# Performance work log

Hardware: AMD Instinct MI355X
Metric: run time of the kernel (lower is better)

## Reference

```python
import jax, jax.numpy as jnp
import numpy as np

DIM = 128
NUM_HEADS = 4
HEAD_DIM = DIM // NUM_HEADS
WH, WW = 7, 7
N_TOK = WH * WW
LAMBDA_K = 1.0
TEMP_MAX = 4.0


def _relative_position_index(wh, ww):
    coords = np.stack(np.meshgrid(np.arange(wh), np.arange(ww), indexing='ij'))  # [2,wh,ww]
    flat = coords.reshape(2, -1)                         # [2,N]
    rel = flat[:, :, None] - flat[:, None, :]            # [2,N,N]
    rel = rel.transpose(1, 2, 0).copy()                  # [N,N,2]
    rel[:, :, 0] += wh - 1
    rel[:, :, 1] += ww - 1
    rel[:, :, 0] *= 2 * ww - 1
    return rel.sum(-1).astype(np.int32)                  # [N,N]


def setup_inputs() -> dict:
    key = jax.random.key(0)
    ks = jax.random.split(key, 10)
    B = 4096
    x = jax.random.normal(ks[0], (B, N_TOK, DIM), dtype=jnp.float32)
    token_u_temp = jax.random.normal(ks[1], (B, N_TOK), dtype=jnp.float32)
    token_u_bias = jax.random.normal(ks[2], (B, N_TOK), dtype=jnp.float32)
    token_gate = jax.random.uniform(ks[3], (B, NUM_HEADS, N_TOK), dtype=jnp.float32)
    qkv_w = jax.random.normal(ks[4], (3 * DIM, DIM), dtype=jnp.float32) * (DIM ** -0.5)
    qkv_b = jax.random.normal(ks[5], (3 * DIM,), dtype=jnp.float32) * 0.02
    proj_w = jax.random.normal(ks[6], (DIM, DIM), dtype=jnp.float32) * (DIM ** -0.5)
    proj_b = jax.random.normal(ks[7], (DIM,), dtype=jnp.float32) * 0.02
    rel_table = jax.random.normal(ks[8], ((2 * WH - 1) * (2 * WW - 1), NUM_HEADS), dtype=jnp.float32) * 0.02
    rel_index = jnp.asarray(_relative_position_index(WH, WW))
    return {
        'x': x, 'token_u_temp': token_u_temp, 'token_u_bias': token_u_bias,
        'token_gate': token_gate, 'qkv_w': qkv_w, 'qkv_b': qkv_b,
        'proj_w': proj_w, 'proj_b': proj_b, 'rel_table': rel_table,
        'rel_index': rel_index,
    }


def reference(x, token_u_temp, token_u_bias, token_gate, qkv_w, qkv_b, proj_w, proj_b, rel_table, rel_index):
    B, N, C = x.shape
    qkv = x @ qkv_w.T + qkv_b                             # [B,N,3C]
    qkv = qkv.reshape(B, N, 3, NUM_HEADS, HEAD_DIM).transpose(2, 0, 3, 1, 4)
    q, k, v = qkv[0], qkv[1], qkv[2]                      # [B,H,N,hd]
    # per-token temperature scaling of q
    T = 0.1 + TEMP_MAX * jax.nn.sigmoid(token_u_temp)     # [B,N]
    q = q / T[:, None, :, None]
    # gathered relative-position bias + per-key bias penalty
    bias = rel_table[rel_index.reshape(-1)].reshape(N, N, NUM_HEADS)
    bias = bias.transpose(2, 0, 1)[None]                  # [1,H,N,N]
    uB = jax.nn.relu(token_u_bias)                        # [B,N]
    mask = bias - LAMBDA_K * uB[:, None, None, :]         # [B,H,N,N]
    scores = jnp.einsum('bhnd,bhmd->bhnm', q, k) * (HEAD_DIM ** -0.5) + mask
    attn = jax.nn.softmax(scores, axis=-1)
    out = jnp.einsum('bhnm,bhmd->bhnd', attn, v)          # [B,H,N,hd]
    out = out * token_gate[:, :, :, None]                 # per-token, per-head gate
    out = out.transpose(0, 2, 1, 3).reshape(B, N, C)
    return out @ proj_w.T + proj_b
```

## Files before the change

kernel.cpp:

```cpp
#include <hip/hip_runtime.h>

typedef short s8v __attribute__((ext_vector_type(8)));
typedef float f4v __attribute__((ext_vector_type(4)));

#define NTOK 49
#define LDS_Q    0
#define LDS_K    6468
#define LDS_RT   12936
#define LDS_UB   12985
#define LDS_GATE 13034
#define LDS_TOT  13230

#define WS_BIAS_OFF 262144

__device__ __forceinline__ unsigned short f2bf(float f){
    unsigned x = __float_as_uint(f);
    x += 0x7fffu + ((x >> 16) & 1u);
    return (unsigned short)(x >> 16);
}
__device__ __forceinline__ void split8t(const float* f, s8v& hi, s8v& lo){
    #pragma unroll
    for (int j = 0; j < 8; ++j){
        unsigned u = __float_as_uint(f[j]);
        hi[j] = (short)(u >> 16);
        float r = f[j] - __uint_as_float(u & 0xffff0000u);
        lo[j] = (short)(__float_as_uint(r) >> 16);
    }
}

__global__ void prep_kernel(const float* __restrict__ qkv_w, const float* __restrict__ proj_w,
                            const float* __restrict__ rel_table, const int* __restrict__ rel_index,
                            void* __restrict__ ws){
    int i = blockIdx.x * 256 + threadIdx.x;
    unsigned short* qh = (unsigned short*)ws;
    unsigned short* ql = qh + 49152;
    unsigned short* ph = (unsigned short*)((char*)ws + 196608);
    unsigned short* pl = (unsigned short*)((char*)ws + 229376);
    float* biasT = (float*)((char*)ws + WS_BIAS_OFF);
    if (i < 49152){
        float v = qkv_w[i];
        unsigned u = __float_as_uint(v);
        qh[i] = (unsigned short)(u >> 16);
        ql[i] = (unsigned short)(__float_as_uint(v - __uint_as_float(u & 0xffff0000u)) >> 16);
    } else if (i < 65536){
        int j = i - 49152;
        float v = proj_w[j];
        unsigned u = __float_as_uint(v);
        ph[j] = (unsigned short)(u >> 16);
        pl[j] = (unsigned short)(__float_as_uint(v - __uint_as_float(u & 0xffff0000u)) >> 16);
    } else if (i < 75140){
        int j = i - 65536;
        int h = j / 2401, r = j % 2401;
        biasT[h*2401 + r] = rel_table[rel_index[r]*4 + h];
    }
}

#define MFMA(a,b,c) __builtin_amdgcn_mfma_f32_16x16x32_bf16((a),(b),(c),0,0,0)

__global__ __launch_bounds__(256, 3)
void win_attn(const float* __restrict__ x, const float* __restrict__ u_temp,
              const float* __restrict__ u_bias, const float* __restrict__ gate,
              const float* __restrict__ qkv_b, const float* __restrict__ proj_b,
              const void* __restrict__ ws, float* __restrict__ out)
{
    __shared__ float sm[LDS_TOT];
    const int b = blockIdx.x, tid = threadIdx.x;
    const int l  = tid & 63;
    const int w  = __builtin_amdgcn_readfirstlane(tid >> 6);
    const int lc = l & 15, q4 = l >> 4;

    if (tid < NTOK){
        float u  = u_temp[b*NTOK + tid];
        float sg = 1.f / (1.f + __expf(-u));
        sm[LDS_RT + tid] = 0.17677669529663687f / (0.1f + 4.f*sg);
        float ub = u_bias[b*NTOK + tid];
        sm[LDS_UB + tid] = ub > 0.f ? ub : 0.f;
    }
    if (tid < 196) sm[LDS_GATE + tid] = gate[b*196 + tid];
    __syncthreads();

    const unsigned short* qkh = (const unsigned short*)ws;
    const unsigned short* qkl = qkh + 49152;

    f4v vhold[2][4];
    #pragma unroll
    for (int mp = 0; mp < 2; ++mp){
        s8v ah[2][4], al[2][4];
        #pragma unroll
        for (int m2 = 0; m2 < 2; ++m2){
            int row = (mp*2 + m2)*16 + lc; if (row > 48) row = 48;
            const float* xp = x + ((size_t)b*NTOK + row)*128 + q4*8;
            #pragma unroll
            for (int kf = 0; kf < 4; ++kf){
                float xv[8];
                float4 t0 = *(const float4*)(xp + kf*32);
                float4 t1 = *(const float4*)(xp + kf*32 + 4);
                xv[0]=t0.x; xv[1]=t0.y; xv[2]=t0.z; xv[3]=t0.w;
                xv[4]=t1.x; xv[5]=t1.y; xv[6]=t1.z; xv[7]=t1.w;
                split8t(xv, ah[m2][kf], al[m2][kf]);
            }
        }
        #pragma unroll
        for (int g = 0; g < 3; ++g){
            #pragma unroll
            for (int t = 0; t < 2; ++t){
                int nt  = (g==0 ? 2*w : (g==1 ? 8+2*w : 16+2*w)) + t;
                int col = nt*16 + lc;
                s8v bh[4], bl[4];
                #pragma unroll
                for (int kf = 0; kf < 4; ++kf){
                    int off = col*128 + kf*32 + q4*8;
                    bh[kf] = *(const s8v*)(qkh + off);
                    bl[kf] = *(const s8v*)(qkl + off);
                }
                float bia = qkv_b[col];
                #pragma unroll
                for (int m2 = 0; m2 < 2; ++m2){
                    f4v acc = {bia, bia, bia, bia};
                    #pragma unroll
                    for (int kf = 0; kf < 4; ++kf){
                        acc = MFMA(ah[m2][kf], bh[kf], acc);
                        acc = MFMA(ah[m2][kf], bl[kf], acc);
                        acc = MFMA(al[m2][kf], bh[kf], acc);
                    }
                    int mt = mp*2 + m2;
                    if (g == 2){
                        vhold[t][mt] = acc;
                    } else {
                        #pragma unroll
                        for (int r = 0; r < 4; ++r){
                            int row = mt*16 + q4*4 + r;
                            if (row < NTOK){
                                if (g == 0) sm[LDS_Q + row*132 + col] = acc[r] * sm[LDS_RT + row];
                                else        sm[LDS_K + row*132 + (col - 128)] = acc[r];
                            }
                        }
                    }
                }
            }
        }
    }

    s8v Kh[4], Kl[4], Qh[4], Ql[4];
    #pragma unroll
    for (int t = 0; t < 4; ++t){
        int row = 16*t + lc; if (row > 48) row = 48;
        float fv[8];
        {
            const float* p = &sm[LDS_K + row*132 + w*32 + q4*8];
            float4 a0 = *(const float4*)p; float4 a1 = *(const float4*)(p + 4);
            fv[0]=a0.x; fv[1]=a0.y; fv[2]=a0.z; fv[3]=a0.w;
            fv[4]=a1.x; fv[5]=a1.y; fv[6]=a1.z; fv[7]=a1.w;
            split8t(fv, Kh[t], Kl[t]);
        }
        {
            const float* p = &sm[LDS_Q + row*132 + w*32 + q4*8];
            float4 a0 = *(const float4*)p; float4 a1 = *(const float4*)(p + 4);
            fv[0]=a0.x; fv[1]=a0.y; fv[2]=a0.z; fv[3]=a0.w;
            fv[4]=a1.x; fv[5]=a1.y; fv[6]=a1.z; fv[7]=a1.w;
            split8t(fv, Qh[t], Ql[t]);
        }
    }

    const float* biasT = (const float*)((const char*)ws + WS_BIAS_OFF);
    unsigned short* P = (unsigned short*)sm;
    #pragma unroll
    for (int nt = 0; nt < 4; ++nt){
        int qy = nt*16 + lc;
        int qyc = qy > 48 ? 48 : qy;
        f4v S[4];
        #pragma unroll
        for (int mt = 0; mt < 4; ++mt){
            f4v a;
            #pragma unroll
            for (int r = 0; r < 4; ++r){
                int ky = mt*16 + q4*4 + r; if (ky > 48) ky = 48;
                a[r] = biasT[w*2401 + qyc*49 + ky] - sm[LDS_UB + ky];
            }
            a = MFMA(Kh[mt], Qh[nt], a);
            a = MFMA(Kh[mt], Ql[nt], a);
            a = MFMA(Kl[mt], Qh[nt], a);
            S[mt] = a;
        }
        #pragma unroll
        for (int r = 0; r < 4; ++r){
            int ky = 48 + q4*4 + r;
            if (ky >= NTOK) S[3][r] = -1e30f;
        }
        float mx = -3e38f;
        #pragma unroll
        for (int mt = 0; mt < 4; ++mt)
            #pragma unroll
            for (int r = 0; r < 4; ++r) mx = fmaxf(mx, S[mt][r]);
        mx = fmaxf(mx, __shfl_xor(mx, 16));
        mx = fmaxf(mx, __shfl_xor(mx, 32));
        float sum = 0.f;
        #pragma unroll
        for (int mt = 0; mt < 4; ++mt)
            #pragma unroll
            for (int r = 0; r < 4; ++r){
                float e = __expf(S[mt][r] - mx);
                S[mt][r] = e; sum += e;
            }
        sum += __shfl_xor(sum, 16);
        sum += __shfl_xor(sum, 32);
        float rs = 1.f / sum;
        if (qy < NTOK){
            #pragma unroll
            for (int mt = 0; mt < 4; ++mt)
                #pragma unroll
                for (int r = 0; r < 4; ++r){
                    int ky = mt*16 + q4*4 + r;
                    P[(qy*132 + w*32)*2 + (((ky>>3) ^ (qy&7)) << 3) + (ky&7)] = f2bf(S[mt][r] * rs);
                }
        }
    }

    #pragma unroll
    for (int t = 0; t < 2; ++t)
        #pragma unroll
        for (int mt = 0; mt < 4; ++mt)
            #pragma unroll
            for (int r = 0; r < 4; ++r){
                int row = mt*16 + q4*4 + r;
                if (row < NTOK) sm[LDS_K + row*132 + w*32 + t*16 + lc] = vhold[t][mt][r];
            }

    s8v Pa[4][2];
    #pragma unroll
    for (int mt = 0; mt < 4; ++mt)
        #pragma unroll
        for (int kf = 0; kf < 2; ++kf){
            int qy = mt*16 + lc; if (qy > 48) qy = 48;
            int ch = (4*kf + q4) ^ (qy & 7);
            Pa[mt][kf] = *(const s8v*)(P + (qy*132 + w*32)*2 + ch*8);
        }
    s8v Vb[2][2];
    #pragma unroll
    for (int t = 0; t < 2; ++t)
        #pragma unroll
        for (int kf = 0; kf < 2; ++kf){
            #pragma unroll
            for (int j = 0; j < 8; ++j){
                int key = kf*32 + q4*8 + j; if (key > 48) key = 48;
                Vb[t][kf][j] = (short)(__float_as_uint(sm[LDS_K + key*132 + w*32 + t*16 + lc]) >> 16);
            }
        }
    f4v O[4][2];
    #pragma unroll
    for (int mt = 0; mt < 4; ++mt)
        #pragma unroll
        for (int t = 0; t < 2; ++t){
            f4v o = {0.f, 0.f, 0.f, 0.f};
            o = MFMA(Pa[mt][0], Vb[t][0], o);
            o = MFMA(Pa[mt][1], Vb[t][1], o);
            O[mt][t] = o;
        }

    #pragma unroll
    for (int mt = 0; mt < 4; ++mt)
        #pragma unroll
        for (int t = 0; t < 2; ++t)
            #pragma unroll
            for (int r = 0; r < 4; ++r){
                int row = mt*16 + q4*4 + r;
                if (row < NTOK){
                    float vg = O[mt][t][r] * sm[LDS_GATE + w*49 + row];
                    unsigned u = __float_as_uint(vg);
                    float res = vg - __uint_as_float(u & 0xffff0000u);
                    char* bp = (char*)sm + (LDS_K + row*132 + w*32)*4;
                    ((unsigned short*)bp)[t*16 + lc]        = (unsigned short)(u >> 16);
                    ((unsigned short*)(bp + 64))[t*16 + lc] = (unsigned short)(__float_as_uint(res) >> 16);
                }
            }
    __syncthreads();

    const unsigned short* ph = (const unsigned short*)((const char*)ws + 196608);
    const unsigned short* pl = (const unsigned short*)((const char*)ws + 229376);
    s8v Bh[2][4], Bl[2][4];
    #pragma unroll
    for (int t = 0; t < 2; ++t){
        int col = (2*w + t)*16 + lc;
        #pragma unroll
        for (int kf = 0; kf < 4; ++kf){
            int off = col*128 + kf*32 + q4*8;
            Bh[t][kf] = *(const s8v*)(ph + off);
            Bl[t][kf] = *(const s8v*)(pl + off);
        }
    }
    #pragma unroll
    for (int mt = 0; mt < 4; ++mt){
        int row = mt*16 + lc; if (row > 48) row = 48;
        s8v Ah[4], Al[4];
        #pragma unroll
        for (int kf = 0; kf < 4; ++kf){
            const char* bp = (const char*)sm + (LDS_K + row*132 + kf*32)*4;
            Ah[kf] = *(const s8v*)(bp + q4*16);
            Al[kf] = *(const s8v*)(bp + 64 + q4*16);
        }
        #pragma unroll
        for (int t = 0; t < 2; ++t){
            int col = (2*w + t)*16 + lc;
            float bia = proj_b[col];
            f4v acc = {bia, bia, bia, bia};
            #pragma unroll
            for (int kf = 0; kf < 4; ++kf){
                acc = MFMA(Ah[kf], Bh[t][kf], acc);
                acc = MFMA(Ah[kf], Bl[t][kf], acc);
                acc = MFMA(Al[kf], Bh[t][kf], acc);
            }
            #pragma unroll
            for (int r = 0; r < 4; ++r){
                int r2 = mt*16 + q4*4 + r;
                if (r2 < NTOK) out[((size_t)b*NTOK + r2)*128 + col] = acc[r];
            }
        }
    }
}

extern "C" void kernel_launch(void* const* d_in, const int* in_sizes, int n_in,
                              void* d_out, int out_size, void* d_ws, size_t ws_size,
                              hipStream_t stream) {
    const float* x  = (const float*)d_in[0];
    const float* ut = (const float*)d_in[1];
    const float* ub = (const float*)d_in[2];
    const float* tg = (const float*)d_in[3];
    const float* qw = (const float*)d_in[4];
    const float* qb = (const float*)d_in[5];
    const float* pw = (const float*)d_in[6];
    const float* pb = (const float*)d_in[7];
    const float* rt = (const float*)d_in[8];
    const int*   ri = (const int*)d_in[9];
    float* o = (float*)d_out;
    const int B = in_sizes[0] / (NTOK * 128);

    prep_kernel<<<294, 256, 0, stream>>>(qw, pw, rt, ri, d_ws);
    win_attn<<<B, 256, 0, stream>>>(x, ut, ub, tg, qb, pb, d_ws, o);
}
```

Before: 496.8 us.

## Double-buffer QKV weight loads, transpose bias table, hoist proj weight loads

```diff
diff --git a/kernel.cpp b/kernel.cpp
--- a/kernel.cpp
+++ b/kernel.cpp
@@ -51,13 +51,13 @@
     } else if (i < 75140){
         int j = i - 65536;
         int h = j / 2401, r = j % 2401;
-        biasT[h*2401 + r] = rel_table[rel_index[r]*4 + h];
+        biasT[h*2401 + (r % 49)*49 + (r / 49)] = rel_table[rel_index[r]*4 + h];
     }
 }
 
 #define MFMA(a,b,c) __builtin_amdgcn_mfma_f32_16x16x32_bf16((a),(b),(c),0,0,0)
 
-__global__ __launch_bounds__(256, 3)
+__global__ __launch_bounds__(256, 2)
 void win_attn(const float* __restrict__ x, const float* __restrict__ u_temp,
               const float* __restrict__ u_bias, const float* __restrict__ gate,
               const float* __restrict__ qkv_b, const float* __restrict__ proj_b,
@@ -100,40 +100,54 @@
                 split8t(xv, ah[m2][kf], al[m2][kf]);
             }
         }
-        #pragma unroll
-        for (int g = 0; g < 3; ++g){
-            #pragma unroll
-            for (int t = 0; t < 2; ++t){
-                int nt  = (g==0 ? 2*w : (g==1 ? 8+2*w : 16+2*w)) + t;
-                int col = nt*16 + lc;
-                s8v bh[4], bl[4];
+        s8v bhA[4], blA[4], bhB[4], blB[4];
+        {
+            int col = (2*w)*16 + lc;
+            #pragma unroll
+            for (int kf = 0; kf < 4; ++kf){
+                int off = col*128 + kf*32 + q4*8;
+                bhA[kf] = *(const s8v*)(qkh + off);
+                blA[kf] = *(const s8v*)(qkl + off);
+            }
+        }
+        #pragma unroll
+        for (int idx = 0; idx < 6; ++idx){
+            const int g = idx >> 1, t = idx & 1;
+            int nt  = (g==0 ? 2*w : (g==1 ? 8+2*w : 16+2*w)) + t;
+            int col = nt*16 + lc;
+            if (idx < 5){
+                const int g2 = (idx+1) >> 1, t2 = (idx+1) & 1;
+                int nt2  = (g2==0 ? 2*w : (g2==1 ? 8+2*w : 16+2*w)) + t2;
+                int col2 = nt2*16 + lc;
                 #pragma unroll
                 for (int kf = 0; kf < 4; ++kf){
-                    int off = col*128 + kf*32 + q4*8;
-                    bh[kf] = *(const s8v*)(qkh + off);
-                    bl[kf] = *(const s8v*)(qkl + off);
-                }
-                float bia = qkv_b[col];
+                    int off = col2*128 + kf*32 + q4*8;
+                    if (idx & 1){ bhA[kf] = *(const s8v*)(qkh + off); blA[kf] = *(const s8v*)(qkl + off); }
+                    else        { bhB[kf] = *(const s8v*)(qkh + off); blB[kf] = *(const s8v*)(qkl + off); }
+                }
+            }
+            float bia = qkv_b[col];
+            #pragma unroll
+            for (int m2 = 0; m2 < 2; ++m2){
+                f4v acc = {bia, bia, bia, bia};
                 #pragma unroll
-                for (int m2 = 0; m2 < 2; ++m2){
-                    f4v acc = {bia, bia, bia, bia};
+                for (int kf = 0; kf < 4; ++kf){
+                    s8v bh = (idx & 1) ? bhB[kf] : bhA[kf];
+                    s8v bl = (idx & 1) ? blB[kf] : blA[kf];
+                    acc = MFMA(ah[m2][kf], bh, acc);
+                    acc = MFMA(ah[m2][kf], bl, acc);
+                    acc = MFMA(al[m2][kf], bh, acc);
+                }
+                int mt = mp*2 + m2;
+                if (g == 2){
+                    vhold[t][mt] = acc;
+                } else {
                     #pragma unroll
-                    for (int kf = 0; kf < 4; ++kf){
-                        acc = MFMA(ah[m2][kf], bh[kf], acc);
-                        acc = MFMA(ah[m2][kf], bl[kf], acc);
-                        acc = MFMA(al[m2][kf], bh[kf], acc);
-                    }
-                    int mt = mp*2 + m2;
-                    if (g == 2){
-                        vhold[t][mt] = acc;
-                    } else {
-                        #pragma unroll
-                        for (int r = 0; r < 4; ++r){
-                            int row = mt*16 + q4*4 + r;
-                            if (row < NTOK){
-                                if (g == 0) sm[LDS_Q + row*132 + col] = acc[r] * sm[LDS_RT + row];
-                                else        sm[LDS_K + row*132 + (col - 128)] = acc[r];
-                            }
+                    for (int r = 0; r < 4; ++r){
+                        int row = mt*16 + q4*4 + r;
+                        if (row < NTOK){
+                            if (g == 0) sm[LDS_Q + row*132 + col] = acc[r] * sm[LDS_RT + row];
+                            else        sm[LDS_K + row*132 + (col - 128)] = acc[r];
                         }
                     }
                 }
@@ -175,7 +189,7 @@
             #pragma unroll
             for (int r = 0; r < 4; ++r){
                 int ky = mt*16 + q4*4 + r; if (ky > 48) ky = 48;
-                a[r] = biasT[w*2401 + qyc*49 + ky] - sm[LDS_UB + ky];
+                a[r] = biasT[w*2401 + ky*49 + qyc] - sm[LDS_UB + ky];
             }
             a = MFMA(Kh[mt], Qh[nt], a);
             a = MFMA(Kh[mt], Ql[nt], a);
@@ -256,6 +270,22 @@
             o = MFMA(Pa[mt][1], Vb[t][1], o);
             O[mt][t] = o;
         }
+
+    const unsigned short* ph = (const unsigned short*)((const char*)ws + 196608);
+    const unsigned short* pl = (const unsigned short*)((const char*)ws + 229376);
+    s8v Bh[2][4], Bl[2][4];
+    float biaP[2];
+    #pragma unroll
+    for (int t = 0; t < 2; ++t){
+        int col = (2*w + t)*16 + lc;
+        #pragma unroll
+        for (int kf = 0; kf < 4; ++kf){
+            int off = col*128 + kf*32 + q4*8;
+            Bh[t][kf] = *(const s8v*)(ph + off);
+            Bl[t][kf] = *(const s8v*)(pl + off);
+        }
+        biaP[t] = proj_b[col];
+    }
 
     #pragma unroll
     for (int mt = 0; mt < 4; ++mt)
@@ -275,19 +305,6 @@
             }
     __syncthreads();
 
-    const unsigned short* ph = (const unsigned short*)((const char*)ws + 196608);
-    const unsigned short* pl = (const unsigned short*)((const char*)ws + 229376);
-    s8v Bh[2][4], Bl[2][4];
-    #pragma unroll
-    for (int t = 0; t < 2; ++t){
-        int col = (2*w + t)*16 + lc;
-        #pragma unroll
-        for (int kf = 0; kf < 4; ++kf){
-            int off = col*128 + kf*32 + q4*8;
-            Bh[t][kf] = *(const s8v*)(ph + off);
-            Bl[t][kf] = *(const s8v*)(pl + off);
-        }
-    }
     #pragma unroll
     for (int mt = 0; mt < 4; ++mt){
         int row = mt*16 + lc; if (row > 48) row = 48;
@@ -301,8 +318,7 @@
         #pragma unroll
         for (int t = 0; t < 2; ++t){
             int col = (2*w + t)*16 + lc;
-            float bia = proj_b[col];
-            f4v acc = {bia, bia, bia, bia};
+            f4v acc = {biaP[t], biaP[t], biaP[t], biaP[t]};
             #pragma unroll
             for (int kf = 0; kf < 4; ++kf){
                 acc = MFMA(Ah[kf], Bh[t][kf], acc);
```

After: 439.7 us. 1.13x faster.
